# Kernel optimization log

Measured on AMD Instinct MI355X. Metric: run time of the kernel, lower is better.

The kernel has to match this reference:

```python
import jax, jax.numpy as jnp
import numpy as np

N = 100000   # nodes
E = 1200000  # edges
F_IN = 16    # input node features
H = 64       # hidden dim (hard-coded in GinNet)
G = 1024     # graphs in the batch
BN_EPS = 1e-5


def setup_inputs() -> dict:
    key = jax.random.key(0)
    ks = jax.random.split(key, 16)

    def dense(k, shape):
        return (jax.random.normal(k, shape, jnp.float32) * (1.0 / np.sqrt(shape[0]))).astype(jnp.float32)

    x = jax.random.normal(ks[0], (N, F_IN), jnp.float32)
    edge_index = jax.random.randint(ks[1], (2, E), 0, N)
    batch = jnp.sort(jax.random.randint(ks[2], (N,), 0, G))

    inp = {
        'x': x, 'edge_index': edge_index, 'batch': batch,
        # GIN layer 1 (MLP F_IN->H->H, eps, BN affine)
        'W1a': dense(ks[3], (F_IN, H)), 'b1a': jnp.zeros((H,), jnp.float32),
        'W1b': dense(ks[4], (H, H)),    'b1b': jnp.zeros((H,), jnp.float32),
        'eps1': jnp.zeros((), jnp.float32), 'g1': jnp.ones((H,), jnp.float32), 'be1': jnp.zeros((H,), jnp.float32),
        # GIN layer 2
        'W2a': dense(ks[5], (H, H)), 'b2a': jnp.zeros((H,), jnp.float32),
        'W2b': dense(ks[6], (H, H)), 'b2b': jnp.zeros((H,), jnp.float32),
        'eps2': jnp.zeros((), jnp.float32), 'g2': jnp.ones((H,), jnp.float32), 'be2': jnp.zeros((H,), jnp.float32),
        # GIN layer 3
        'W3a': dense(ks[7], (H, H)), 'b3a': jnp.zeros((H,), jnp.float32),
        'W3b': dense(ks[8], (H, H)), 'b3b': jnp.zeros((H,), jnp.float32),
        'eps3': jnp.zeros((), jnp.float32), 'g3': jnp.ones((H,), jnp.float32), 'be3': jnp.zeros((H,), jnp.float32),
        # readout MLP
        'Wf1': dense(ks[9], (H, 10)), 'bf1': jnp.zeros((10,), jnp.float32),
        'Wf2': dense(ks[10], (10, 1)), 'bf2': jnp.zeros((1,), jnp.float32),
    }
    return inp


def _gin_bn(x, edge_index, eps, Wa, ba, Wb, bb, gamma, beta):
    # GINConv: out = MLP((1+eps)*x + sum_{j->i} x_j)
    msgs = x[edge_index[0]]                                      # [E, d] gather
    aggr = jax.ops.segment_sum(msgs, edge_index[1], num_segments=N)  # [N, d] scatter-add
    h = (1.0 + eps) * x + aggr
    h = jnp.maximum(h @ Wa + ba, 0.0) @ Wb + bb                  # Linear-ReLU-Linear
    h = jnp.maximum(h, 0.0)                                      # F.relu after conv
    # BatchNorm1d in training mode: batch statistics (biased var)
    mu = h.mean(axis=0)
    var = h.var(axis=0)
    return gamma * (h - mu) * jax.lax.rsqrt(var + BN_EPS) + beta


def reference(x, edge_index, batch,
              W1a, b1a, W1b, b1b, eps1, g1, be1,
              W2a, b2a, W2b, b2b, eps2, g2, be2,
              W3a, b3a, W3b, b3b, eps3, g3, be3,
              Wf1, bf1, Wf2, bf2):
    h = _gin_bn(x, edge_index, eps1, W1a, b1a, W1b, b1b, g1, be1)
    h = _gin_bn(h, edge_index, eps2, W2a, b2a, W2b, b2b, g2, be2)
    h = _gin_bn(h, edge_index, eps3, W3a, b3a, W3b, b3b, g3, be3)
    # global_mean_pool over graph ids
    sums = jax.ops.segment_sum(h, batch, num_segments=G)                     # [G, H]
    cnt = jax.ops.segment_sum(jnp.ones((N,), jnp.float32), batch, num_segments=G)
    pooled = sums / jnp.maximum(cnt, 1.0)[:, None]
    h = jnp.maximum(pooled @ Wf1 + bf1, 0.0)
    return h @ Wf2 + bf2  # [G, 1]
```

## Files before the change

kernel.cpp:

```cpp
#include <hip/hip_runtime.h>
#include <hip/hip_bf16.h>


#define HD 64
#define NBLK 256
#define BSH 9
#define SREP 8

typedef unsigned short u16;
typedef unsigned int u32;

__device__ __forceinline__ float bf2f(u16 u) {
    return __uint_as_float(((u32)u) << 16);
}
__device__ __forceinline__ u16 f2bf(float f) {
    u32 u = __float_as_uint(f);
    u32 r = 0x7FFFu + ((u >> 16) & 1u);
    return (u16)((u + r) >> 16);
}

__global__ void hist_kernel(const int* __restrict__ ei, int* __restrict__ ghist, int E, int C) {
    __shared__ int lh[256];
    int b = blockIdx.x, tid = threadIdx.x;
    lh[tid] = 0;
    __syncthreads();
    int beg = b * C, end = min(beg + C, E);
    for (int i = beg + tid; i < end; i += 256) atomicAdd(&lh[ei[E + i] >> BSH], 1);
    __syncthreads();
    ghist[b * 256 + tid] = lh[tid];
}

__global__ void colscan_kernel(int* __restrict__ ghist, int* __restrict__ total) {
    __shared__ int s[256];
    int k = blockIdx.x, b = threadIdx.x;
    int v = ghist[b * 256 + k];
    s[b] = v;
    __syncthreads();
    for (int off = 1; off < 256; off <<= 1) {
        int u = (b >= off) ? s[b - off] : 0;
        __syncthreads();
        s[b] += u;
        __syncthreads();
    }
    ghist[b * 256 + k] = s[b] - v;
    if (b == 255) total[k] = s[255];
}

__global__ void base_kernel(const int* __restrict__ total, int* __restrict__ bbase, int NBUCK) {
    __shared__ int s[256];
    int t = threadIdx.x;
    int v = (t < NBUCK) ? total[t] : 0;
    s[t] = v;
    __syncthreads();
    for (int off = 1; off < 256; off <<= 1) {
        int u = (t >= off) ? s[t - off] : 0;
        __syncthreads();
        s[t] += u;
        __syncthreads();
    }
    if (t == 0) bbase[0] = 0;
    bbase[t + 1] = s[t];
}

__global__ void scatter_kernel(const int* __restrict__ ei, const int* __restrict__ ghist,
                               const int* __restrict__ bbase, int* __restrict__ bpack,
                               int E, int C) {
    __shared__ int lcur[256];
    int b = blockIdx.x, tid = threadIdx.x;
    lcur[tid] = bbase[tid] + ghist[b * 256 + tid];
    __syncthreads();
    int beg = b * C, end = min(beg + C, E);
    for (int i = beg + tid; i < end; i += 256) {
        int src = ei[i], dst = ei[E + i];
        int pos = atomicAdd(&lcur[dst >> BSH], 1);
        bpack[pos] = src | ((dst & 511) << 17);
    }
}

__global__ void csrbuild_kernel(const int* __restrict__ bpack, const int* __restrict__ bbase,
                                int* __restrict__ row_start, int* __restrict__ csr, int N) {
    __shared__ int h[512], s[512], lc[512];
    int k = blockIdx.x, tid = threadIdx.x;
    int beg = bbase[k], end = bbase[k + 1];
    h[tid] = 0; h[tid + 256] = 0;
    __syncthreads();
    for (int i = beg + tid; i < end; i += 256) atomicAdd(&h[(bpack[i] >> 17) & 511], 1);
    __syncthreads();
    s[tid] = h[tid]; s[tid + 256] = h[tid + 256];
    __syncthreads();
    for (int off = 1; off < 512; off <<= 1) {
        int v0 = (tid >= off) ? s[tid - off] : 0;
        int t1 = tid + 256;
        int v1 = (t1 >= off) ? s[t1 - off] : 0;
        __syncthreads();
        s[tid] += v0; s[t1] += v1;
        __syncthreads();
    }
    int e0 = s[tid] - h[tid], e1 = s[tid + 256] - h[tid + 256];
    lc[tid] = e0; lc[tid + 256] = e1;
    int n0 = (k << BSH) + tid, n1 = (k << BSH) + tid + 256;
    if (n0 < N) row_start[n0] = beg + e0;
    if (n1 < N) row_start[n1] = beg + e1;
    if (k == gridDim.x - 1 && tid == 0) row_start[N] = end;
    __syncthreads();
    for (int i = beg + tid; i < end; i += 256) {
        int v = bpack[i];
        int pos = beg + atomicAdd(&lc[(v >> 17) & 511], 1);
        csr[pos] = v & 0x1FFFF;
    }
}

__global__ void gather64_kernel(const u16* __restrict__ x, const int* __restrict__ rs,
                                const int* __restrict__ csr, float* __restrict__ aggr, int N) {
    int lane = threadIdx.x & 63;
    int l4 = lane & 15;
    int wave = (blockIdx.x * blockDim.x + threadIdx.x) >> 6;
    int n = wave * 4 + (lane >> 4);
    if (n >= N) return;
    int beg = rs[n], end = rs[n + 1];
    const u16* xb = x + (size_t)l4 * 4;
    float a0x = 0, a0y = 0, a0z = 0, a0w = 0;
    float a1x = 0, a1y = 0, a1z = 0, a1w = 0;
    float a2x = 0, a2y = 0, a2z = 0, a2w = 0;
    float a3x = 0, a3y = 0, a3z = 0, a3w = 0;
    for (int base = beg; base < end; base += 16) {
        int cnt = end - base; if (cnt > 16) cnt = 16;
        int e = (l4 < cnt) ? csr[base + l4] : 0;
        int j = 0;
        for (; j + 4 <= cnt; j += 4) {
            int s0 = __shfl(e, j + 0, 16);
            int s1 = __shfl(e, j + 1, 16);
            int s2 = __shfl(e, j + 2, 16);
            int s3 = __shfl(e, j + 3, 16);
            ushort4 u0 = *(const ushort4*)(xb + (size_t)s0 * 64);
            ushort4 u1 = *(const ushort4*)(xb + (size_t)s1 * 64);
            ushort4 u2 = *(const ushort4*)(xb + (size_t)s2 * 64);
            ushort4 u3 = *(const ushort4*)(xb + (size_t)s3 * 64);
            a0x += bf2f(u0.x); a0y += bf2f(u0.y); a0z += bf2f(u0.z); a0w += bf2f(u0.w);
            a1x += bf2f(u1.x); a1y += bf2f(u1.y); a1z += bf2f(u1.z); a1w += bf2f(u1.w);
            a2x += bf2f(u2.x); a2y += bf2f(u2.y); a2z += bf2f(u2.z); a2w += bf2f(u2.w);
            a3x += bf2f(u3.x); a3y += bf2f(u3.y); a3z += bf2f(u3.z); a3w += bf2f(u3.w);
        }
        for (; j < cnt; j++) {
            int s = __shfl(e, j, 16);
            ushort4 u = *(const ushort4*)(xb + (size_t)s * 64);
            a0x += bf2f(u.x); a0y += bf2f(u.y); a0z += bf2f(u.z); a0w += bf2f(u.w);
        }
    }
    float4 o;
    o.x = (a0x + a1x) + (a2x + a3x);
    o.y = (a0y + a1y) + (a2y + a3y);
    o.z = (a0z + a1z) + (a2z + a3z);
    o.w = (a0w + a1w) + (a2w + a3w);
    *reinterpret_cast<float4*>(aggr + (size_t)n * 64 + l4 * 4) = o;
}

__global__ void gather16_kernel(const float* __restrict__ x, const int* __restrict__ rs,
                                const int* __restrict__ csr, float* __restrict__ aggr, int N) {
    int lane = threadIdx.x & 63;
    int l4 = lane & 3;
    int wave = (blockIdx.x * blockDim.x + threadIdx.x) >> 6;
    int n = wave * 16 + (lane >> 2);
    if (n >= N) return;
    int beg = rs[n], end = rs[n + 1];
    const float* xb = x + (size_t)l4 * 4;
    float a0x = 0, a0y = 0, a0z = 0, a0w = 0;
    float a1x = 0, a1y = 0, a1z = 0, a1w = 0;
    float a2x = 0, a2y = 0, a2z = 0, a2w = 0;
    float a3x = 0, a3y = 0, a3z = 0, a3w = 0;
    for (int base = beg; base < end; base += 4) {
        int cnt = end - base; if (cnt > 4) cnt = 4;
        int e = (l4 < cnt) ? csr[base + l4] : 0;
        if (cnt == 4) {
            int s0 = __shfl(e, 0, 4);
            int s1 = __shfl(e, 1, 4);
            int s2 = __shfl(e, 2, 4);
            int s3 = __shfl(e, 3, 4);
            float4 v0 = *(const float4*)(xb + (size_t)s0 * 16);
            float4 v1 = *(const float4*)(xb + (size_t)s1 * 16);
            float4 v2 = *(const float4*)(xb + (size_t)s2 * 16);
            float4 v3 = *(const float4*)(xb + (size_t)s3 * 16);
            a0x += v0.x; a0y += v0.y; a0z += v0.z; a0w += v0.w;
            a1x += v1.x; a1y += v1.y; a1z += v1.z; a1w += v1.w;
            a2x += v2.x; a2y += v2.y; a2z += v2.z; a2w += v2.w;
            a3x += v3.x; a3y += v3.y; a3z += v3.z; a3w += v3.w;
        } else {
            for (int j = 0; j < cnt; j++) {
                int s = __shfl(e, j, 4);
                float4 v = *(const float4*)(xb + (size_t)s * 16);
                a0x += v.x; a0y += v.y; a0z += v.z; a0w += v.w;
            }
        }
    }
    float4 o;
    o.x = (a0x + a1x) + (a2x + a3x);
    o.y = (a0y + a1y) + (a2y + a3y);
    o.z = (a0z + a1z) + (a2z + a3z);
    o.w = (a0w + a1w) + (a2w + a3w);
    *reinterpret_cast<float4*>(aggr + (size_t)n * 16 + l4 * 4) = o;
}

template <int DIN, bool AFF, bool POOL>
__launch_bounds__(256)
__global__ void fused_mlp_kernel(const void* __restrict__ xin_, const float* __restrict__ aggr,
                                 const int* __restrict__ rs, const int* __restrict__ batch,
                                 const float* __restrict__ Wa, const float* __restrict__ ba,
                                 const float* __restrict__ Wb, const float* __restrict__ bb,
                                 const float* __restrict__ epsp,
                                 const float* __restrict__ statsPrev,
                                 const float* __restrict__ gPrev, const float* __restrict__ bePrev,
                                 u16* __restrict__ hout, float* __restrict__ stats,
                                 float* __restrict__ pool, float* __restrict__ cnt, int N) {
    __shared__ float W_s[64 * 64];
    __shared__ float zts[64 * 68];
    __shared__ float statS[128];
    __shared__ float degS[64];
    __shared__ float aS[64], cS[64], uS[64];

    const int tid = threadIdx.x;
    const int tc = tid & 15;
    const int tn = tid >> 4;
    const float* xinF = (const float*)xin_;
    const u16*   xinB = (const u16*)xin_;

    int blockBase = blockIdx.x * 64;

    ushort4 xuP[4]; float4 avP[4];
    float4  xvP, av16P;
    if (DIN == 64) {
#pragma unroll
        for (int i = 0; i < 4; ++i) {
            int node = blockBase + tn * 4 + i;
            xuP[i] = make_ushort4(0, 0, 0, 0);
            avP[i] = make_float4(0, 0, 0, 0);
            if (node < N) {
                xuP[i] = *(const ushort4*)&xinB[(size_t)node * 64 + tc * 4];
                avP[i] = *(const float4*)&aggr[(size_t)node * 64 + tc * 4];
            }
        }
    } else {
        int node = blockBase + tn * 4 + (tc >> 2);
        xvP = make_float4(0, 0, 0, 0);
        av16P = make_float4(0, 0, 0, 0);
        if (node < N) {
            xvP = *(const float4*)&xinF[(size_t)node * 16 + (tc & 3) * 4];
            av16P = *(const float4*)&aggr[(size_t)node * 16 + (tc & 3) * 4];
        }
    }
    float wbR[16];
#pragma unroll
    for (int i = 0; i < 16; ++i) wbR[i] = Wb[tid + i * 256];

    if (AFF) {
        if (tid < 64) {
            float invN = 1.0f / (float)N;
            float s0 = 0, s1 = 0;
#pragma unroll
            for (int r = 0; r < SREP; ++r) {
                s0 += statsPrev[r * 128 + tid];
                s1 += statsPrev[r * 128 + 64 + tid];
            }
            float mu = s0 * invN;
            float var = s1 * invN - mu * mu;
            float inv = rsqrtf(var + 1e-5f);
            float a = gPrev[tid] * inv;
            aS[tid] = a;
            cS[tid] = bePrev[tid] - mu * a;
        }
        __syncthreads();
        for (int i = tid; i < DIN * 64; i += 256) W_s[i] = aS[i >> 6] * Wa[i];
        if (tid < 64) {
            float s = 0.0f;
            for (int k = 0; k < 64; k++) s = fmaf(cS[k], Wa[k * 64 + tid], s);
            uS[tid] = s;
        }
    } else {
        for (int i = tid; i < DIN * 64; i += 256) W_s[i] = Wa[i];
    }
    if (tid < 128) statS[tid] = 0.0f;
    const float e1 = 1.0f + epsp[0];
    if (AFF && tid < 64) {
        int node = blockBase + tid;
        degS[tid] = (node < N) ? (float)(rs[node + 1] - rs[node]) : 0.0f;
    }

    float4 t4;
    t4 = *(const float4*)&ba[tc * 4];
    const float bav[4] = {t4.x, t4.y, t4.z, t4.w};
    t4 = *(const float4*)&bb[tc * 4];
    const float bbv[4] = {t4.x, t4.y, t4.z, t4.w};

    float sv[4] = {0, 0, 0, 0}, qv[4] = {0, 0, 0, 0};

    float zr[4][4];
    if (DIN == 64) {
#pragma unroll
        for (int i = 0; i < 4; ++i) {
            zr[i][0] = fmaf(e1, bf2f(xuP[i].x), avP[i].x);
            zr[i][1] = fmaf(e1, bf2f(xuP[i].y), avP[i].y);
            zr[i][2] = fmaf(e1, bf2f(xuP[i].z), avP[i].z);
            zr[i][3] = fmaf(e1, bf2f(xuP[i].w), avP[i].w);
        }
#pragma unroll
        for (int j = 0; j < 4; ++j) {
            float4 w = {zr[0][j], zr[1][j], zr[2][j], zr[3][j]};
            *(float4*)&zts[(tc * 4 + j) * 68 + tn * 4] = w;
        }
    } else {
        zr[0][0] = fmaf(e1, xvP.x, av16P.x);
        zr[0][1] = fmaf(e1, xvP.y, av16P.y);
        zr[0][2] = fmaf(e1, xvP.z, av16P.z);
        zr[0][3] = fmaf(e1, xvP.w, av16P.w);
#pragma unroll
        for (int j = 0; j < 4; ++j)
            zts[((tc & 3) * 4 + j) * 68 + tn * 4 + (tc >> 2)] = zr[0][j];
    }
    __syncthreads();
    float uv[4] = {0, 0, 0, 0};
    if (AFF) { uv[0] = uS[tc * 4]; uv[1] = uS[tc * 4 + 1]; uv[2] = uS[tc * 4 + 2]; uv[3] = uS[tc * 4 + 3]; }
    float dg[4];
    if (AFF) {
#pragma unroll
        for (int i = 0; i < 4; ++i) dg[i] = e1 + degS[tn * 4 + i];
    }
    float ac[4][4];
#pragma unroll
    for (int i = 0; i < 4; ++i)
#pragma unroll
        for (int j = 0; j < 4; ++j)
            ac[i][j] = AFF ? fmaf(dg[i], uv[j], bav[j]) : bav[j];
#pragma unroll 8
    for (int k = 0; k < DIN; ++k) {
        float4 zv = *(const float4*)&zts[k * 68 + tn * 4];
        float4 wv = *(const float4*)&W_s[k * 64 + tc * 4];
        const float zf[4] = {zv.x, zv.y, zv.z, zv.w};
        const float wf[4] = {wv.x, wv.y, wv.z, wv.w};
#pragma unroll
        for (int i = 0; i < 4; ++i)
#pragma unroll
            for (int j = 0; j < 4; ++j)
                ac[i][j] = fmaf(zf[i], wf[j], ac[i][j]);
    }
#pragma unroll
    for (int i = 0; i < 4; ++i)
#pragma unroll
        for (int j = 0; j < 4; ++j)
            ac[i][j] = fmaxf(ac[i][j], 0.0f);
    __syncthreads();
#pragma unroll
    for (int j = 0; j < 4; ++j) {
        float4 w = {ac[0][j], ac[1][j], ac[2][j], ac[3][j]};
        *(float4*)&zts[(tc * 4 + j) * 68 + tn * 4] = w;
    }
#pragma unroll
    for (int i = 0; i < 16; ++i) W_s[tid + i * 256] = wbR[i];
    __syncthreads();
    float hc[4][4];
#pragma unroll
    for (int i = 0; i < 4; ++i)
#pragma unroll
        for (int j = 0; j < 4; ++j)
            hc[i][j] = bbv[j];
#pragma unroll 8
    for (int k = 0; k < 64; ++k) {
        float4 tv = *(const float4*)&zts[k * 68 + tn * 4];
        float4 wv = *(const float4*)&W_s[k * 64 + tc * 4];
        const float tf[4] = {tv.x, tv.y, tv.z, tv.w};
        const float wf[4] = {wv.x, wv.y, wv.z, wv.w};
#pragma unroll
        for (int i = 0; i < 4; ++i)
#pragma unroll
            for (int j = 0; j < 4; ++j)
                hc[i][j] = fmaf(tf[i], wf[j], hc[i][j]);
    }
    if (POOL) {
        int curg = -1; float p0 = 0, p1 = 0, p2 = 0, p3 = 0; int run = 0;
#pragma unroll
        for (int i = 0; i < 4; ++i) {
            int node = blockBase + tn * 4 + i;
            if (node < N) {
                float o0 = fmaxf(hc[i][0], 0.0f), o1 = fmaxf(hc[i][1], 0.0f);
                float o2 = fmaxf(hc[i][2], 0.0f), o3 = fmaxf(hc[i][3], 0.0f);
                sv[0] += o0; sv[1] += o1; sv[2] += o2; sv[3] += o3;
                qv[0] += o0 * o0; qv[1] += o1 * o1; qv[2] += o2 * o2; qv[3] += o3 * o3;
                int gid = batch[node];
                if (gid != curg) {
                    if (curg >= 0) {
                        unsafeAtomicAdd(&pool[(size_t)curg * 64 + tc * 4 + 0], p0);
                        unsafeAtomicAdd(&pool[(size_t)curg * 64 + tc * 4 + 1], p1);
                        unsafeAtomicAdd(&pool[(size_t)curg * 64 + tc * 4 + 2], p2);
                        unsafeAtomicAdd(&pool[(size_t)curg * 64 + tc * 4 + 3], p3);
                        if (tc == 0) unsafeAtomicAdd(&cnt[curg], (float)run);
                    }
                    curg = gid; p0 = p1 = p2 = p3 = 0.0f; run = 0;
                }
                p0 += o0; p1 += o1; p2 += o2; p3 += o3; run++;
            }
        }
        if (curg >= 0) {
            unsafeAtomicAdd(&pool[(size_t)curg * 64 + tc * 4 + 0], p0);
            unsafeAtomicAdd(&pool[(size_t)curg * 64 + tc * 4 + 1], p1);
            unsafeAtomicAdd(&pool[(size_t)curg * 64 + tc * 4 + 2], p2);
            unsafeAtomicAdd(&pool[(size_t)curg * 64 + tc * 4 + 3], p3);
            if (tc == 0) unsafeAtomicAdd(&cnt[curg], (float)run);
        }
    } else {
#pragma unroll
        for (int i = 0; i < 4; ++i) {
            int node = blockBase + tn * 4 + i;
            if (node < N) {
                float o0 = fmaxf(hc[i][0], 0.0f), o1 = fmaxf(hc[i][1], 0.0f);
                float o2 = fmaxf(hc[i][2], 0.0f), o3 = fmaxf(hc[i][3], 0.0f);
                ushort4 ob = {f2bf(o0), f2bf(o1), f2bf(o2), f2bf(o3)};
                *(ushort4*)&hout[(size_t)node * 64 + tc * 4] = ob;
                sv[0] += o0; sv[1] += o1; sv[2] += o2; sv[3] += o3;
                qv[0] += o0 * o0; qv[1] += o1 * o1; qv[2] += o2 * o2; qv[3] += o3 * o3;
            }
        }
    }
#pragma unroll
    for (int off = 16; off < 64; off <<= 1) {
#pragma unroll
        for (int j = 0; j < 4; ++j) {
            sv[j] += __shfl_xor(sv[j], off);
            qv[j] += __shfl_xor(qv[j], off);
        }
    }
    if ((tid & 63) < 16) {
#pragma unroll
        for (int j = 0; j < 4; ++j) {
            atomicAdd(&statS[tc * 4 + j], sv[j]);
            atomicAdd(&statS[64 + tc * 4 + j], qv[j]);
        }
    }
    __syncthreads();
    if (tid < 128) unsafeAtomicAdd(&stats[(blockIdx.x & (SREP - 1)) * 128 + tid], statS[tid]);
}

__global__ void readout_kernel(const float* __restrict__ pool, const float* __restrict__ cnt,
                               const float* __restrict__ stats, const float* __restrict__ g3,
                               const float* __restrict__ be3,
                               const float* __restrict__ Wf1, const float* __restrict__ bf1,
                               const float* __restrict__ Wf2, const float* __restrict__ bf2,
                               float* __restrict__ out, int N) {
    int gb = blockIdx.x;
    int t = threadIdx.x;
    float invN = 1.0f / (float)N;
    float s0 = 0, s1 = 0;
#pragma unroll
    for (int r = 0; r < SREP; ++r) {
        s0 += stats[r * 128 + t];
        s1 += stats[r * 128 + 64 + t];
    }
    float mu = s0 * invN;
    float var = s1 * invN - mu * mu;
    float inv = rsqrtf(var + 1e-5f);
    float a = g3[t] * inv;
    float c = be3[t] - mu * a;
    float cn = cnt[gb];
    float p = (cn > 0.0f) ? (a * (pool[(size_t)gb * 64 + t] / cn) + c) : 0.0f;
    float o = 0.0f;
#pragma unroll
    for (int j = 0; j < 10; j++) {
        float part = p * Wf1[t * 10 + j];
#pragma unroll
        for (int off = 32; off > 0; off >>= 1) part += __shfl_down(part, off);
        float z = fmaxf(part + bf1[j], 0.0f);
        o = fmaf(z, Wf2[j], o);
    }
    if (t == 0) out[gb] = o + bf2[0];
}

extern "C" void kernel_launch(void* const* d_in, const int* in_sizes, int n_in,
                              void* d_out, int out_size, void* d_ws, size_t ws_size,
                              hipStream_t stream) {
    const float* x      = (const float*)d_in[0];
    const int*   ei     = (const int*)d_in[1];
    const int*   batch  = (const int*)d_in[2];
    const float* W1a = (const float*)d_in[3];  const float* b1a = (const float*)d_in[4];
    const float* W1b = (const float*)d_in[5];  const float* b1b = (const float*)d_in[6];
    const float* e1  = (const float*)d_in[7];  const float* g1  = (const float*)d_in[8];
    const float* be1 = (const float*)d_in[9];
    const float* W2a = (const float*)d_in[10]; const float* b2a = (const float*)d_in[11];
    const float* W2b = (const float*)d_in[12]; const float* b2b = (const float*)d_in[13];
    const float* e2  = (const float*)d_in[14]; const float* g2  = (const float*)d_in[15];
    const float* be2 = (const float*)d_in[16];
    const float* W3a = (const float*)d_in[17]; const float* b3a = (const float*)d_in[18];
    const float* W3b = (const float*)d_in[19]; const float* b3b = (const float*)d_in[20];
    const float* e3  = (const float*)d_in[21]; const float* g3  = (const float*)d_in[22];
    const float* be3 = (const float*)d_in[23];
    const float* Wf1 = (const float*)d_in[24]; const float* bf1 = (const float*)d_in[25];
    const float* Wf2 = (const float*)d_in[26]; const float* bf2 = (const float*)d_in[27];

    const int N = in_sizes[2];
    const int E = in_sizes[1] / 2;
    const int G = out_size;
    const int NBUCK = (N + 511) >> BSH;
    const int C = (E + NBLK - 1) / NBLK;

    int* csr       = (int*)d_ws;
    int* row_start = csr + E;
    int* bpack     = row_start + N + 64;
    int* ghist     = bpack + E;
    int* total     = ghist + NBLK * 256;
    int* bbase     = total + 256;
    float* stats   = (float*)(bbase + 272);
    float* pool    = stats + 3 * SREP * 128;
    float* cnt     = pool + (size_t)G * HD;
    float* aggr    = cnt + G;
    size_t NH = (size_t)N * HD;
    u16* hA        = (u16*)(aggr + NH);
    u16* hB        = hA + NH;

    const int TB = 256;
    int fusedGrid = (N + 63) / 64;
    size_t zeroBytes = (size_t)(3 * SREP * 128 + (size_t)G * HD + G) * sizeof(float);

    hipMemsetAsync(stats, 0, zeroBytes, stream);
    hist_kernel<<<NBLK, 256, 0, stream>>>(ei, ghist, E, C);
    colscan_kernel<<<NBUCK, 256, 0, stream>>>(ghist, total);
    base_kernel<<<1, 256, 0, stream>>>(total, bbase, NBUCK);
    scatter_kernel<<<NBLK, 256, 0, stream>>>(ei, ghist, bbase, bpack, E, C);
    csrbuild_kernel<<<NBUCK, 256, 0, stream>>>(bpack, bbase, row_start, csr, N);

    gather16_kernel<<<((N + 15) / 16 * 64 + TB - 1) / TB, TB, 0, stream>>>(x, row_start, csr, aggr, N);
    fused_mlp_kernel<16, false, false><<<fusedGrid, TB, 0, stream>>>(
        x, aggr, row_start, batch, W1a, b1a, W1b, b1b, e1,
        nullptr, nullptr, nullptr, hA, stats, nullptr, nullptr, N);

    gather64_kernel<<<((N + 3) / 4 * 64 + TB - 1) / TB, TB, 0, stream>>>(hA, row_start, csr, aggr, N);
    fused_mlp_kernel<64, true, false><<<fusedGrid, TB, 0, stream>>>(
        hA, aggr, row_start, batch, W2a, b2a, W2b, b2b, e2,
        stats, g1, be1, hB, stats + SREP * 128, nullptr, nullptr, N);

    gather64_kernel<<<((N + 3) / 4 * 64 + TB - 1) / TB, TB, 0, stream>>>(hB, row_start, csr, aggr, N);
    fused_mlp_kernel<64, true, true><<<fusedGrid, TB, 0, stream>>>(
        hB, aggr, row_start, batch, W3a, b3a, W3b, b3b, e3,
        stats + SREP * 128, g2, be2, hA , stats + 2 * SREP * 128, pool, cnt, N);

    readout_kernel<<<G, 64, 0, stream>>>(pool, cnt, stats + 2 * SREP * 128, g3, be3,
                                         Wf1, bf1, Wf2, bf2, (float*)d_out, N);
}
```

Measured before the change: 383.3 us.

## Make fused MLP kernel persistent with next-tile prefetch and replicated pool buffers

Turns the fused GIN MLP kernel into a grid-stride persistent kernel capped at 1024 blocks. Each block now sets up the weight and BN affine prologue once, keeps Wa in registers, and prefetches the next tile's node features and aggregates while computing the current tile. The global mean-pool accumulators are replicated SREP ways to spread atomic contention, and the readout sums the replicas. The cost is extra registers, an extra barrier and shared-memory rewrite of Wa per tile, and a larger memset.

```diff
diff --git a/kernel.cpp b/kernel.cpp
--- a/kernel.cpp
+++ b/kernel.cpp
@@ -210,7 +210,8 @@
                                  const float* __restrict__ statsPrev,
                                  const float* __restrict__ gPrev, const float* __restrict__ bePrev,
                                  u16* __restrict__ hout, float* __restrict__ stats,
-                                 float* __restrict__ pool, float* __restrict__ cnt, int N) {
+                                 float* __restrict__ pool, float* __restrict__ cnt,
+                                 int N, int G) {
     __shared__ float W_s[64 * 64];
     __shared__ float zts[64 * 68];
     __shared__ float statS[128];
@@ -222,35 +223,44 @@
     const int tn = tid >> 4;
     const float* xinF = (const float*)xin_;
     const u16*   xinB = (const u16*)xin_;
-
-    int blockBase = blockIdx.x * 64;
-
+    constexpr int WAn = DIN / 4;
+
+    const int ntiles = (N + 63) >> 6;
+    const int rep = blockIdx.x & (SREP - 1);
+    float* poolR = POOL ? pool + (size_t)rep * G * 64 : nullptr;
+    float* cntR  = POOL ? cnt + (size_t)rep * G : nullptr;
+
+    int tile = blockIdx.x;
     ushort4 xuP[4]; float4 avP[4];
     float4  xvP, av16P;
-    if (DIN == 64) {
-#pragma unroll
-        for (int i = 0; i < 4; ++i) {
-            int node = blockBase + tn * 4 + i;
-            xuP[i] = make_ushort4(0, 0, 0, 0);
-            avP[i] = make_float4(0, 0, 0, 0);
+    {
+        int blockBase = tile * 64;
+        if (DIN == 64) {
+#pragma unroll
+            for (int i = 0; i < 4; ++i) {
+                int node = blockBase + tn * 4 + i;
+                xuP[i] = make_ushort4(0, 0, 0, 0);
+                avP[i] = make_float4(0, 0, 0, 0);
+                if (node < N) {
+                    xuP[i] = *(const ushort4*)&xinB[(size_t)node * 64 + tc * 4];
+                    avP[i] = *(const float4*)&aggr[(size_t)node * 64 + tc * 4];
+                }
+            }
+        } else {
+            int node = blockBase + tn * 4 + (tc >> 2);
+            xvP = make_float4(0, 0, 0, 0);
+            av16P = make_float4(0, 0, 0, 0);
             if (node < N) {
-                xuP[i] = *(const ushort4*)&xinB[(size_t)node * 64 + tc * 4];
-                avP[i] = *(const float4*)&aggr[(size_t)node * 64 + tc * 4];
-            }
-        }
-    } else {
-        int node = blockBase + tn * 4 + (tc >> 2);
-        xvP = make_float4(0, 0, 0, 0);
-        av16P = make_float4(0, 0, 0, 0);
-        if (node < N) {
-            xvP = *(const float4*)&xinF[(size_t)node * 16 + (tc & 3) * 4];
-            av16P = *(const float4*)&aggr[(size_t)node * 16 + (tc & 3) * 4];
+                xvP = *(const float4*)&xinF[(size_t)node * 16 + (tc & 3) * 4];
+                av16P = *(const float4*)&aggr[(size_t)node * 16 + (tc & 3) * 4];
+            }
         }
     }
     float wbR[16];
 #pragma unroll
     for (int i = 0; i < 16; ++i) wbR[i] = Wb[tid + i * 256];
 
+    float waR[WAn];
     if (AFF) {
         if (tid < 64) {
             float invN = 1.0f / (float)N;
@@ -268,21 +278,22 @@
             cS[tid] = bePrev[tid] - mu * a;
         }
         __syncthreads();
-        for (int i = tid; i < DIN * 64; i += 256) W_s[i] = aS[i >> 6] * Wa[i];
+#pragma unroll
+        for (int i = 0; i < WAn; ++i) {
+            int idx = tid + i * 256;
+            waR[i] = aS[idx >> 6] * Wa[idx];
+        }
         if (tid < 64) {
             float s = 0.0f;
             for (int k = 0; k < 64; k++) s = fmaf(cS[k], Wa[k * 64 + tid], s);
             uS[tid] = s;
         }
     } else {
-        for (int i = tid; i < DIN * 64; i += 256) W_s[i] = Wa[i];
+#pragma unroll
+        for (int i = 0; i < WAn; ++i) waR[i] = Wa[tid + i * 256];
     }
     if (tid < 128) statS[tid] = 0.0f;
     const float e1 = 1.0f + epsp[0];
-    if (AFF && tid < 64) {
-        int node = blockBase + tid;
-        degS[tid] = (node < N) ? (float)(rs[node + 1] - rs[node]) : 0.0f;
-    }
 
     float4 t4;
     t4 = *(const float4*)&ba[tc * 4];
@@ -291,130 +302,172 @@
     const float bbv[4] = {t4.x, t4.y, t4.z, t4.w};
 
     float sv[4] = {0, 0, 0, 0}, qv[4] = {0, 0, 0, 0};
-
-    float zr[4][4];
-    if (DIN == 64) {
-#pragma unroll
-        for (int i = 0; i < 4; ++i) {
-            zr[i][0] = fmaf(e1, bf2f(xuP[i].x), avP[i].x);
-            zr[i][1] = fmaf(e1, bf2f(xuP[i].y), avP[i].y);
-            zr[i][2] = fmaf(e1, bf2f(xuP[i].z), avP[i].z);
-            zr[i][3] = fmaf(e1, bf2f(xuP[i].w), avP[i].w);
-        }
+    float uv[4] = {0, 0, 0, 0};
+    bool uvLoaded = false;
+
+    for (; tile < ntiles; tile += gridDim.x) {
+        int blockBase = tile * 64;
+        __syncthreads();
+#pragma unroll
+        for (int i = 0; i < WAn; ++i) W_s[tid + i * 256] = waR[i];
+        float zr[4][4];
+        if (DIN == 64) {
+#pragma unroll
+            for (int i = 0; i < 4; ++i) {
+                zr[i][0] = fmaf(e1, bf2f(xuP[i].x), avP[i].x);
+                zr[i][1] = fmaf(e1, bf2f(xuP[i].y), avP[i].y);
+                zr[i][2] = fmaf(e1, bf2f(xuP[i].z), avP[i].z);
+                zr[i][3] = fmaf(e1, bf2f(xuP[i].w), avP[i].w);
+            }
+#pragma unroll
+            for (int j = 0; j < 4; ++j) {
+                float4 w = {zr[0][j], zr[1][j], zr[2][j], zr[3][j]};
+                *(float4*)&zts[(tc * 4 + j) * 68 + tn * 4] = w;
+            }
+        } else {
+            zr[0][0] = fmaf(e1, xvP.x, av16P.x);
+            zr[0][1] = fmaf(e1, xvP.y, av16P.y);
+            zr[0][2] = fmaf(e1, xvP.z, av16P.z);
+            zr[0][3] = fmaf(e1, xvP.w, av16P.w);
+#pragma unroll
+            for (int j = 0; j < 4; ++j)
+                zts[((tc & 3) * 4 + j) * 68 + tn * 4 + (tc >> 2)] = zr[0][j];
+        }
+        if (AFF && tid < 64) {
+            int node = blockBase + tid;
+            degS[tid] = (node < N) ? (float)(rs[node + 1] - rs[node]) : 0.0f;
+        }
+        {
+            int nt = tile + gridDim.x;
+            if (nt < ntiles) {
+                int nb = nt * 64;
+                if (DIN == 64) {
+#pragma unroll
+                    for (int i = 0; i < 4; ++i) {
+                        int node = nb + tn * 4 + i;
+                        ushort4 xu = make_ushort4(0, 0, 0, 0);
+                        float4 av = make_float4(0, 0, 0, 0);
+                        if (node < N) {
+                            xu = *(const ushort4*)&xinB[(size_t)node * 64 + tc * 4];
+                            av = *(const float4*)&aggr[(size_t)node * 64 + tc * 4];
+                        }
+                        xuP[i] = xu; avP[i] = av;
+                    }
+                } else {
+                    int node = nb + tn * 4 + (tc >> 2);
+                    float4 xv = make_float4(0, 0, 0, 0), av = make_float4(0, 0, 0, 0);
+                    if (node < N) {
+                        xv = *(const float4*)&xinF[(size_t)node * 16 + (tc & 3) * 4];
+                        av = *(const float4*)&aggr[(size_t)node * 16 + (tc & 3) * 4];
+                    }
+                    xvP = xv; av16P = av;
+                }
+            }
+        }
+        __syncthreads();
+        if (AFF && !uvLoaded) {
+            uv[0] = uS[tc * 4]; uv[1] = uS[tc * 4 + 1];
+            uv[2] = uS[tc * 4 + 2]; uv[3] = uS[tc * 4 + 3];
+            uvLoaded = true;
+        }
+        float dg[4];
+        if (AFF) {
+#pragma unroll
+            for (int i = 0; i < 4; ++i) dg[i] = e1 + degS[tn * 4 + i];
+        }
+        float ac[4][4];
+#pragma unroll
+        for (int i = 0; i < 4; ++i)
+#pragma unroll
+            for (int j = 0; j < 4; ++j)
+                ac[i][j] = AFF ? fmaf(dg[i], uv[j], bav[j]) : bav[j];
+#pragma unroll 8
+        for (int k = 0; k < DIN; ++k) {
+            float4 zv = *(const float4*)&zts[k * 68 + tn * 4];
+            float4 wv = *(const float4*)&W_s[k * 64 + tc * 4];
+            const float zf[4] = {zv.x, zv.y, zv.z, zv.w};
+            const float wf[4] = {wv.x, wv.y, wv.z, wv.w};
+#pragma unroll
+            for (int i = 0; i < 4; ++i)
+#pragma unroll
+                for (int j = 0; j < 4; ++j)
+                    ac[i][j] = fmaf(zf[i], wf[j], ac[i][j]);
+        }
+#pragma unroll
+        for (int i = 0; i < 4; ++i)
+#pragma unroll
+            for (int j = 0; j < 4; ++j)
+                ac[i][j] = fmaxf(ac[i][j], 0.0f);
+        __syncthreads();
 #pragma unroll
         for (int j = 0; j < 4; ++j) {
-            float4 w = {zr[0][j], zr[1][j], zr[2][j], zr[3][j]};
+            float4 w = {ac[0][j], ac[1][j], ac[2][j], ac[3][j]};
             *(float4*)&zts[(tc * 4 + j) * 68 + tn * 4] = w;
         }
-    } else {
-        zr[0][0] = fmaf(e1, xvP.x, av16P.x);
-        zr[0][1] = fmaf(e1, xvP.y, av16P.y);
-        zr[0][2] = fmaf(e1, xvP.z, av16P.z);
-        zr[0][3] = fmaf(e1, xvP.w, av16P.w);
-#pragma unroll
-        for (int j = 0; j < 4; ++j)
-            zts[((tc & 3) * 4 + j) * 68 + tn * 4 + (tc >> 2)] = zr[0][j];
-    }
-    __syncthreads();
-    float uv[4] = {0, 0, 0, 0};
-    if (AFF) { uv[0] = uS[tc * 4]; uv[1] = uS[tc * 4 + 1]; uv[2] = uS[tc * 4 + 2]; uv[3] = uS[tc * 4 + 3]; }
-    float dg[4];
-    if (AFF) {
-#pragma unroll
-        for (int i = 0; i < 4; ++i) dg[i] = e1 + degS[tn * 4 + i];
-    }
-    float ac[4][4];
-#pragma unroll
-    for (int i = 0; i < 4; ++i)
-#pragma unroll
-        for (int j = 0; j < 4; ++j)
-            ac[i][j] = AFF ? fmaf(dg[i], uv[j], bav[j]) : bav[j];
+#pragma unroll
+        for (int i = 0; i < 16; ++i) W_s[tid + i * 256] = wbR[i];
+        __syncthreads();
+        float hc[4][4];
+#pragma unroll
+        for (int i = 0; i < 4; ++i)
+#pragma unroll
+            for (int j = 0; j < 4; ++j)
+                hc[i][j] = bbv[j];
 #pragma unroll 8
-    for (int k = 0; k < DIN; ++k) {
-        float4 zv = *(const float4*)&zts[k * 68 + tn * 4];
-        float4 wv = *(const float4*)&W_s[k * 64 + tc * 4];
-        const float zf[4] = {zv.x, zv.y, zv.z, zv.w};
-        const float wf[4] = {wv.x, wv.y, wv.z, wv.w};
-#pragma unroll
-        for (int i = 0; i < 4; ++i)
-#pragma unroll
-            for (int j = 0; j < 4; ++j)
-                ac[i][j] = fmaf(zf[i], wf[j], ac[i][j]);
-    }
-#pragma unroll
-    for (int i = 0; i < 4; ++i)
-#pragma unroll
-        for (int j = 0; j < 4; ++j)
-            ac[i][j] = fmaxf(ac[i][j], 0.0f);
-    __syncthreads();
-#pragma unroll
-    for (int j = 0; j < 4; ++j) {
-        float4 w = {ac[0][j], ac[1][j], ac[2][j], ac[3][j]};
-        *(float4*)&zts[(tc * 4 + j) * 68 + tn * 4] = w;
-    }
-#pragma unroll
-    for (int i = 0; i < 16; ++i) W_s[tid + i * 256] = wbR[i];
-    __syncthreads();
-    float hc[4][4];
-#pragma unroll
-    for (int i = 0; i < 4; ++i)
-#pragma unroll
-        for (int j = 0; j < 4; ++j)
-            hc[i][j] = bbv[j];
-#pragma unroll 8
-    for (int k = 0; k < 64; ++k) {
-        float4 tv = *(const float4*)&zts[k * 68 + tn * 4];
-        float4 wv = *(const float4*)&W_s[k * 64 + tc * 4];
-        const float tf[4] = {tv.x, tv.y, tv.z, tv.w};
-        const float wf[4] = {wv.x, wv.y, wv.z, wv.w};
-#pragma unroll
-        for (int i = 0; i < 4; ++i)
-#pragma unroll
-            for (int j = 0; j < 4; ++j)
-                hc[i][j] = fmaf(tf[i], wf[j], hc[i][j]);
-    }
-    if (POOL) {
-        int curg = -1; float p0 = 0, p1 = 0, p2 = 0, p3 = 0; int run = 0;
-#pragma unroll
-        for (int i = 0; i < 4; ++i) {
-            int node = blockBase + tn * 4 + i;
-            if (node < N) {
-                float o0 = fmaxf(hc[i][0], 0.0f), o1 = fmaxf(hc[i][1], 0.0f);
-                float o2 = fmaxf(hc[i][2], 0.0f), o3 = fmaxf(hc[i][3], 0.0f);
-                sv[0] += o0; sv[1] += o1; sv[2] += o2; sv[3] += o3;
-                qv[0] += o0 * o0; qv[1] += o1 * o1; qv[2] += o2 * o2; qv[3] += o3 * o3;
-                int gid = batch[node];
-                if (gid != curg) {
-                    if (curg >= 0) {
-                        unsafeAtomicAdd(&pool[(size_t)curg * 64 + tc * 4 + 0], p0);
-                        unsafeAtomicAdd(&pool[(size_t)curg * 64 + tc * 4 + 1], p1);
-                        unsafeAtomicAdd(&pool[(size_t)curg * 64 + tc * 4 + 2], p2);
-                        unsafeAtomicAdd(&pool[(size_t)curg * 64 + tc * 4 + 3], p3);
-                        if (tc == 0) unsafeAtomicAdd(&cnt[curg], (float)run);
+        for (int k = 0; k < 64; ++k) {
+            float4 tv = *(const float4*)&zts[k * 68 + tn * 4];
+            float4 wv = *(const float4*)&W_s[k * 64 + tc * 4];
+            const float tf[4] = {tv.x, tv.y, tv.z, tv.w};
+            const float wf[4] = {wv.x, wv.y, wv.z, wv.w};
+#pragma unroll
+            for (int i = 0; i < 4; ++i)
+#pragma unroll
+                for (int j = 0; j < 4; ++j)
+                    hc[i][j] = fmaf(tf[i], wf[j], hc[i][j]);
+        }
+        if (POOL) {
+            int curg = -1; float p0 = 0, p1 = 0, p2 = 0, p3 = 0; int run = 0;
+#pragma unroll
+            for (int i = 0; i < 4; ++i) {
+                int node = blockBase + tn * 4 + i;
+                if (node < N) {
+                    float o0 = fmaxf(hc[i][0], 0.0f), o1 = fmaxf(hc[i][1], 0.0f);
+                    float o2 = fmaxf(hc[i][2], 0.0f), o3 = fmaxf(hc[i][3], 0.0f);
+                    sv[0] += o0; sv[1] += o1; sv[2] += o2; sv[3] += o3;
+                    qv[0] += o0 * o0; qv[1] += o1 * o1; qv[2] += o2 * o2; qv[3] += o3 * o3;
+                    int gid = batch[node];
+                    if (gid != curg) {
+                        if (curg >= 0) {
+                            unsafeAtomicAdd(&poolR[(size_t)curg * 64 + tc * 4 + 0], p0);
+                            unsafeAtomicAdd(&poolR[(size_t)curg * 64 + tc * 4 + 1], p1);
+                            unsafeAtomicAdd(&poolR[(size_t)curg * 64 + tc * 4 + 2], p2);
+                            unsafeAtomicAdd(&poolR[(size_t)curg * 64 + tc * 4 + 3], p3);
+                            if (tc == 0) unsafeAtomicAdd(&cntR[curg], (float)run);
+                        }
+                        curg = gid; p0 = p1 = p2 = p3 = 0.0f; run = 0;
                     }
-                    curg = gid; p0 = p1 = p2 = p3 = 0.0f; run = 0;
+                    p0 += o0; p1 += o1; p2 += o2; p3 += o3; run++;
                 }
-                p0 += o0; p1 += o1; p2 += o2; p3 += o3; run++;
-            }
-        }
-        if (curg >= 0) {
-            unsafeAtomicAdd(&pool[(size_t)curg * 64 + tc * 4 + 0], p0);
-            unsafeAtomicAdd(&pool[(size_t)curg * 64 + tc * 4 + 1], p1);
-            unsafeAtomicAdd(&pool[(size_t)curg * 64 + tc * 4 + 2], p2);
-            unsafeAtomicAdd(&pool[(size_t)curg * 64 + tc * 4 + 3], p3);
-            if (tc == 0) unsafeAtomicAdd(&cnt[curg], (float)run);
-        }
-    } else {
-#pragma unroll
-        for (int i = 0; i < 4; ++i) {
-            int node = blockBase + tn * 4 + i;
-            if (node < N) {
-                float o0 = fmaxf(hc[i][0], 0.0f), o1 = fmaxf(hc[i][1], 0.0f);
-                float o2 = fmaxf(hc[i][2], 0.0f), o3 = fmaxf(hc[i][3], 0.0f);
-                ushort4 ob = {f2bf(o0), f2bf(o1), f2bf(o2), f2bf(o3)};
-                *(ushort4*)&hout[(size_t)node * 64 + tc * 4] = ob;
-                sv[0] += o0; sv[1] += o1; sv[2] += o2; sv[3] += o3;
-                qv[0] += o0 * o0; qv[1] += o1 * o1; qv[2] += o2 * o2; qv[3] += o3 * o3;
+            }
+            if (curg >= 0) {
+                unsafeAtomicAdd(&poolR[(size_t)curg * 64 + tc * 4 + 0], p0);
+                unsafeAtomicAdd(&poolR[(size_t)curg * 64 + tc * 4 + 1], p1);
+                unsafeAtomicAdd(&poolR[(size_t)curg * 64 + tc * 4 + 2], p2);
+                unsafeAtomicAdd(&poolR[(size_t)curg * 64 + tc * 4 + 3], p3);
+                if (tc == 0) unsafeAtomicAdd(&cntR[curg], (float)run);
+            }
+        } else {
+#pragma unroll
+            for (int i = 0; i < 4; ++i) {
+                int node = blockBase + tn * 4 + i;
+                if (node < N) {
+                    float o0 = fmaxf(hc[i][0], 0.0f), o1 = fmaxf(hc[i][1], 0.0f);
+                    float o2 = fmaxf(hc[i][2], 0.0f), o3 = fmaxf(hc[i][3], 0.0f);
+                    ushort4 ob = {f2bf(o0), f2bf(o1), f2bf(o2), f2bf(o3)};
+                    *(ushort4*)&hout[(size_t)node * 64 + tc * 4] = ob;
+                    sv[0] += o0; sv[1] += o1; sv[2] += o2; sv[3] += o3;
+                    qv[0] += o0 * o0; qv[1] += o1 * o1; qv[2] += o2 * o2; qv[3] += o3 * o3;
+                }
             }
         }
     }
@@ -434,7 +487,7 @@
         }
     }
     __syncthreads();
-    if (tid < 128) unsafeAtomicAdd(&stats[(blockIdx.x & (SREP - 1)) * 128 + tid], statS[tid]);
+    if (tid < 128) unsafeAtomicAdd(&stats[rep * 128 + tid], statS[tid]);
 }
 
 __global__ void readout_kernel(const float* __restrict__ pool, const float* __restrict__ cnt,
@@ -442,23 +495,24 @@
                                const float* __restrict__ be3,
                                const float* __restrict__ Wf1, const float* __restrict__ bf1,
                                const float* __restrict__ Wf2, const float* __restrict__ bf2,
-                               float* __restrict__ out, int N) {
+                               float* __restrict__ out, int N, int G) {
     int gb = blockIdx.x;
     int t = threadIdx.x;
     float invN = 1.0f / (float)N;
-    float s0 = 0, s1 = 0;
+    float s0 = 0, s1 = 0, ps = 0, cs = 0;
 #pragma unroll
     for (int r = 0; r < SREP; ++r) {
         s0 += stats[r * 128 + t];
         s1 += stats[r * 128 + 64 + t];
+        ps += pool[(size_t)r * G * 64 + (size_t)gb * 64 + t];
+        cs += cnt[(size_t)r * G + gb];
     }
     float mu = s0 * invN;
     float var = s1 * invN - mu * mu;
     float inv = rsqrtf(var + 1e-5f);
     float a = g3[t] * inv;
     float c = be3[t] - mu * a;
-    float cn = cnt[gb];
-    float p = (cn > 0.0f) ? (a * (pool[(size_t)gb * 64 + t] / cn) + c) : 0.0f;
+    float p = (cs > 0.0f) ? (a * (ps / cs) + c) : 0.0f;
     float o = 0.0f;
 #pragma unroll
     for (int j = 0; j < 10; j++) {
@@ -497,6 +551,7 @@
     const int G = out_size;
     const int NBUCK = (N + 511) >> BSH;
     const int C = (E + NBLK - 1) / NBLK;
+    const int ntiles = (N + 63) / 64;
 
     int* csr       = (int*)d_ws;
     int* row_start = csr + E;
@@ -506,15 +561,15 @@
     int* bbase     = total + 256;
     float* stats   = (float*)(bbase + 272);
     float* pool    = stats + 3 * SREP * 128;
-    float* cnt     = pool + (size_t)G * HD;
-    float* aggr    = cnt + G;
+    float* cnt     = pool + (size_t)SREP * G * HD;
+    float* aggr    = cnt + (size_t)SREP * G;
     size_t NH = (size_t)N * HD;
     u16* hA        = (u16*)(aggr + NH);
     u16* hB        = hA + NH;
 
     const int TB = 256;
-    int fusedGrid = (N + 63) / 64;
-    size_t zeroBytes = (size_t)(3 * SREP * 128 + (size_t)G * HD + G) * sizeof(float);
+    int fusedGrid = ntiles < 1024 ? ntiles : 1024;
+    size_t zeroBytes = ((size_t)3 * SREP * 128 + (size_t)SREP * G * HD + (size_t)SREP * G) * sizeof(float);
 
     hipMemsetAsync(stats, 0, zeroBytes, stream);
     hist_kernel<<<NBLK, 256, 0, stream>>>(ei, ghist, E, C);
@@ -526,18 +581,18 @@
     gather16_kernel<<<((N + 15) / 16 * 64 + TB - 1) / TB, TB, 0, stream>>>(x, row_start, csr, aggr, N);
     fused_mlp_kernel<16, false, false><<<fusedGrid, TB, 0, stream>>>(
         x, aggr, row_start, batch, W1a, b1a, W1b, b1b, e1,
-        nullptr, nullptr, nullptr, hA, stats, nullptr, nullptr, N);
+        nullptr, nullptr, nullptr, hA, stats, nullptr, nullptr, N, G);
 
     gather64_kernel<<<((N + 3) / 4 * 64 + TB - 1) / TB, TB, 0, stream>>>(hA, row_start, csr, aggr, N);
     fused_mlp_kernel<64, true, false><<<fusedGrid, TB, 0, stream>>>(
         hA, aggr, row_start, batch, W2a, b2a, W2b, b2b, e2,
-        stats, g1, be1, hB, stats + SREP * 128, nullptr, nullptr, N);
+        stats, g1, be1, hB, stats + SREP * 128, nullptr, nullptr, N, G);
 
     gather64_kernel<<<((N + 3) / 4 * 64 + TB - 1) / TB, TB, 0, stream>>>(hB, row_start, csr, aggr, N);
     fused_mlp_kernel<64, true, true><<<fusedGrid, TB, 0, stream>>>(
         hB, aggr, row_start, batch, W3a, b3a, W3b, b3b, e3,
-        stats + SREP * 128, g2, be2, hA , stats + 2 * SREP * 128, pool, cnt, N);
+        stats + SREP * 128, g2, be2, hA , stats + 2 * SREP * 128, pool, cnt, N, G);
 
     readout_kernel<<<G, 64, 0, stream>>>(pool, cnt, stats + 2 * SREP * 128, g3, be3,
-                                         Wf1, bf1, Wf2, bf2, (float*)d_out, N);
-}
+                                         Wf1, bf1, Wf2, bf2, (float*)d_out, N, G);
+}
```

Result: faster. 371.1 us (-3.2%).
